# Kernel optimization log

Measured on AMD Instinct MI355X. Metric: run time of the kernel, lower is better.

The kernel has to match this reference:

```python
import jax, jax.numpy as jnp
import numpy as np

D_IN = 2048
D_OUT = 2048
NUM_HEADS = 16
NUM_KV_GROUPS = 4
HEAD_DIM = D_OUT // NUM_HEADS          # 128
GROUP_SIZE = NUM_HEADS // NUM_KV_GROUPS  # 4


def setup_inputs() -> dict:
    key = jax.random.key(0)
    ks = jax.random.split(key, 7)
    B, N = 2, 2048
    s = 1.0 / np.sqrt(D_IN)
    return {
        "query": jax.random.normal(ks[0], (B, N, D_IN), dtype=jnp.float32),
        "key":   jax.random.normal(ks[1], (B, N, D_IN), dtype=jnp.float32),
        "value": jax.random.normal(ks[2], (B, N, D_IN), dtype=jnp.float32),
        # weights stored as (in, out); y = x @ W  (equivalent to torch Linear, no bias)
        "Wq": jax.random.normal(ks[3], (D_IN, D_OUT), dtype=jnp.float32) * s,
        "Wk": jax.random.normal(ks[4], (D_IN, NUM_KV_GROUPS * HEAD_DIM), dtype=jnp.float32) * s,
        "Wv": jax.random.normal(ks[5], (D_IN, NUM_KV_GROUPS * HEAD_DIM), dtype=jnp.float32) * s,
        "Wo": jax.random.normal(ks[6], (D_OUT, D_OUT), dtype=jnp.float32) * s,
    }


def reference(query, key, value, Wq, Wk, Wv, Wo):
    B, N, _ = query.shape
    S = key.shape[1]
    # projections
    q = (query @ Wq).reshape(B, N, NUM_HEADS, HEAD_DIM)        # b n (h g) d
    k = (key   @ Wk).reshape(B, S, NUM_KV_GROUPS, HEAD_DIM)
    v = (value @ Wv).reshape(B, S, NUM_KV_GROUPS, HEAD_DIM)
    # b h n d layouts
    q = q.transpose(0, 2, 1, 3)                                # (B, H, N, d)
    k = k.transpose(0, 2, 1, 3)                                # (B, Hk, S, d)
    v = v.transpose(0, 2, 1, 3)                                # (B, Hk, S, d)
    # rearrange 'b (h g) n d -> b g h n d' with g = GROUP_SIZE, h = NUM_KV_GROUPS
    q = q.reshape(B, NUM_KV_GROUPS, GROUP_SIZE, N, HEAD_DIM).transpose(0, 2, 1, 3, 4)  # (B, g, h, N, d)
    # NOTE: the original module applies NO 1/sqrt(d) scaling — kept faithful.
    scores = jnp.einsum('bghnd,bhsd->bghns', q, k)             # (B, g, h, N, S)
    weights = jax.nn.softmax(scores, axis=-1)                  # dropout p=0.0 -> identity
    ctx = jnp.einsum('bghns,bhsd->bghnd', weights, v)          # (B, g, h, N, d)
    ctx = ctx.transpose(0, 3, 1, 2, 4).reshape(B, N, D_OUT)    # b n (g h d)
    attn_output = ctx @ Wo
    attn_output_weights = weights.reshape(B * NUM_HEADS, N, S) # (b g h) t s
    return attn_output, attn_output_weights
```

## Files before the change

### kernel.cpp

```cpp
#include <hip/hip_runtime.h>
#include <hip/hip_bf16.h>
#include <stdint.h>


typedef __attribute__((ext_vector_type(4))) float f32x4;
typedef __attribute__((ext_vector_type(8))) short short8;

#define GLDS(gsrc, ldst) __builtin_amdgcn_global_load_lds( \
  (const __attribute__((address_space(1))) void*)(gsrc),   \
  (__attribute__((address_space(3))) void*)(ldst), 16, 0, 0)

__device__ __forceinline__ f32x4 MFMA(short8 a, short8 b, f32x4 c) {
  return __builtin_amdgcn_mfma_f32_16x16x32_bf16(a, b, c, 0, 0, 0);
}

__device__ __forceinline__ unsigned short f2bf(float f) {
  union { float f; uint32_t u; } v; v.f = f;
  uint32_t r = v.u + 0x7FFFu + ((v.u >> 16) & 1u);
  return (unsigned short)(r >> 16);
}
__device__ __forceinline__ float bf2f(unsigned short h) {
  union { uint32_t u; float f; } v; v.u = ((uint32_t)h) << 16;
  return v.f;
}
__device__ __forceinline__ int swz128(int r, int byte) {
  return r * 128 + (byte ^ ((r & 7) << 4));
}
__device__ __forceinline__ int swz256(int r, int byte) {
  return r * 256 + ((byte & 15) | ((((byte >> 4) & 15) ^ (r & 15)) << 4));
}

__global__ __launch_bounds__(1024) void transpose_split(
    const float* __restrict__ W, unsigned short* __restrict__ Thi,
    unsigned short* __restrict__ Tlo, int K, int C) {
  __shared__ float tile[32][33];
  int c0 = blockIdx.x * 32, k0 = blockIdx.y * 32;
  int tx = threadIdx.x, ty = threadIdx.y;
  tile[ty][tx] = W[(size_t)(k0 + ty) * C + c0 + tx];
  __syncthreads();
  float f = tile[tx][ty];
  size_t o = (size_t)(c0 + ty) * K + k0 + tx;
  unsigned short hi = f2bf(f);
  Thi[o] = hi;
  if (Tlo) Tlo[o] = f2bf(f - bf2f(hi));
}

template <int MODE>
__global__ __launch_bounds__(256, 2) void proj_kernel(
    const float* __restrict__ X,
    const unsigned short* __restrict__ WTh,
    const unsigned short* __restrict__ WTl,
    unsigned short* __restrict__ Oh,
    unsigned short* __restrict__ Ol,
    int Ctot) {
  __shared__ __align__(16) unsigned short xh[128 * 64];
  __shared__ __align__(16) unsigned short xl[128 * 64];
  __shared__ __align__(16) unsigned short wh[128 * 64];
  __shared__ __align__(16) unsigned short wl[128 * 64];
  const int t = threadIdx.x;
  const int n0 = blockIdx.x * 128, m0 = blockIdx.y * 128;
  const int wid = t >> 6, lane = t & 63;
  const int wm = (wid >> 1) * 64, wn = (wid & 1) * 64;
  f32x4 acc[4][4] = {};
  for (int k0 = 0; k0 < 2048; k0 += 64) {
    #pragma unroll
    for (int i = 0; i < 8; ++i) {
      int e = (i * 256 + t) * 4;
      int r = e >> 6, c = e & 63;
      float4 f = *(const float4*)(X + (size_t)(m0 + r) * 2048 + k0 + c);
      unsigned short h0 = f2bf(f.x), h1 = f2bf(f.y), h2 = f2bf(f.z), h3 = f2bf(f.w);
      int off = swz128(r, c * 2);
      *(uint2*)((char*)xh + off) = make_uint2((unsigned)h0 | ((unsigned)h1 << 16),
                                              (unsigned)h2 | ((unsigned)h3 << 16));
      if (MODE == 0) {
        unsigned short l0 = f2bf(f.x - bf2f(h0)), l1 = f2bf(f.y - bf2f(h1));
        unsigned short l2 = f2bf(f.z - bf2f(h2)), l3 = f2bf(f.w - bf2f(h3));
        *(uint2*)((char*)xl + off) = make_uint2((unsigned)l0 | ((unsigned)l1 << 16),
                                                (unsigned)l2 | ((unsigned)l3 << 16));
      }
    }
    #pragma unroll
    for (int i = 0; i < 4; ++i) {
      int L = i * 4096 + t * 16;
      int r = L >> 7;
      int ss = ((L >> 4) & 7) ^ (r & 7);
      GLDS(WTh + (size_t)(n0 + r) * 2048 + k0 + ss * 8, (char*)wh + i * 4096 + wid * 1024);
      if (MODE == 0)
        GLDS(WTl + (size_t)(n0 + r) * 2048 + k0 + ss * 8, (char*)wl + i * 4096 + wid * 1024);
    }
    __syncthreads();
    #pragma unroll
    for (int ks = 0; ks < 2; ++ks) {
      const int kb = ks * 64 + (lane >> 4) * 16;
      short8 ah[4], al[4], bh[4], bl[4];
      #pragma unroll
      for (int mi = 0; mi < 4; ++mi) {
        int r = wm + mi * 16 + (lane & 15);
        ah[mi] = *(const short8*)((char*)xh + swz128(r, kb));
        if (MODE == 0) al[mi] = *(const short8*)((char*)xl + swz128(r, kb));
      }
      #pragma unroll
      for (int ni = 0; ni < 4; ++ni) {
        int r = wn + ni * 16 + (lane & 15);
        bh[ni] = *(const short8*)((char*)wh + swz128(r, kb));
        if (MODE == 0) bl[ni] = *(const short8*)((char*)wl + swz128(r, kb));
      }
      #pragma unroll
      for (int mi = 0; mi < 4; ++mi)
        #pragma unroll
        for (int ni = 0; ni < 4; ++ni) {
          acc[mi][ni] = MFMA(ah[mi], bh[ni], acc[mi][ni]);
          if (MODE == 0) {
            acc[mi][ni] = MFMA(al[mi], bh[ni], acc[mi][ni]);
            acc[mi][ni] = MFMA(ah[mi], bl[ni], acc[mi][ni]);
          }
        }
    }
    __syncthreads();
  }
  #pragma unroll
  for (int mi = 0; mi < 4; ++mi)
    #pragma unroll
    for (int ni = 0; ni < 4; ++ni)
      #pragma unroll
      for (int rg = 0; rg < 4; ++rg) {
        int row = m0 + wm + mi * 16 + (lane >> 4) * 4 + rg;
        int col = n0 + wn + ni * 16 + (lane & 15);
        float y = acc[mi][ni][rg];
        if (MODE == 0) {
          unsigned short hi = f2bf(y);
          size_t o = (size_t)row * Ctot + col;
          Oh[o] = hi;
          Ol[o] = f2bf(y - bf2f(hi));
        } else {
          Oh[((size_t)(row >> 11) * 512 + col) * 2048 + (row & 2047)] = f2bf(y);
        }
      }
}

__global__ __launch_bounds__(256, 2) void attn_kernel(
    const unsigned short* __restrict__ Qh, const unsigned short* __restrict__ Ql,
    const unsigned short* __restrict__ Kh, const unsigned short* __restrict__ Kl,
    const unsigned short* __restrict__ VT,
    float* __restrict__ Wout,
    unsigned short* __restrict__ Ctx) {
  __shared__ __align__(16) char lds[65536];
  const int bp = blockIdx.y;
  const int b = bp >> 4, p = bp & 15;
  const int hq = (p & 3) * 4 + (p >> 2);
  const int kv = p & 3;
  const int n0 = blockIdx.x * 128;
  const int t = threadIdx.x, wid = t >> 6, lane = t & 63;
  const int wrow = wid * 32;

  {
    size_t qbase = ((size_t)(b * 2048 + n0)) * 2048 + hq * 128;
    #pragma unroll
    for (int i = 0; i < 8; ++i) {
      int L = i * 4096 + t * 16;
      int r = L >> 8;
      int ss = ((L >> 4) & 15) ^ (r & 15);
      GLDS(Qh + qbase + (size_t)r * 2048 + ss * 8, lds + i * 4096 + wid * 1024);
      GLDS(Ql + qbase + (size_t)r * 2048 + ss * 8, lds + 32768 + i * 4096 + wid * 1024);
    }
  }
  __syncthreads();
  short8 qa_h[2][4], qa_l[2][4];
  #pragma unroll
  for (int mf = 0; mf < 2; ++mf)
    #pragma unroll
    for (int ks = 0; ks < 4; ++ks) {
      int r = wrow + mf * 16 + (lane & 15);
      int byte = ks * 64 + (lane >> 4) * 16;
      qa_h[mf][ks] = *(const short8*)(lds + swz256(r, byte));
      qa_l[mf][ks] = *(const short8*)(lds + 32768 + swz256(r, byte));
    }
  __syncthreads();

  const size_t kbase = (size_t)b * 2048 * 512 + kv * 128;
  float lp[2][4];
  #pragma unroll
  for (int mf = 0; mf < 2; ++mf)
    #pragma unroll
    for (int rg = 0; rg < 4; ++rg) lp[mf][rg] = 0.f;

  for (int s0 = 0; s0 < 2048; s0 += 64) {
    #pragma unroll
    for (int i = 0; i < 4; ++i) {
      int L = i * 4096 + t * 16;
      int r = L >> 8;
      int ss = ((L >> 4) & 15) ^ (r & 15);
      GLDS(Kh + kbase + (size_t)(s0 + r) * 512 + ss * 8, lds + i * 4096 + wid * 1024);
      GLDS(Kl + kbase + (size_t)(s0 + r) * 512 + ss * 8, lds + 16384 + i * 4096 + wid * 1024);
    }
    __syncthreads();
    f32x4 sc[2][4] = {};
    #pragma unroll
    for (int sf = 0; sf < 4; ++sf)
      #pragma unroll
      for (int ks = 0; ks < 4; ++ks) {
        int r = sf * 16 + (lane & 15);
        int byte = ks * 64 + (lane >> 4) * 16;
        short8 bh = *(const short8*)(lds + swz256(r, byte));
        short8 bl = *(const short8*)(lds + 16384 + swz256(r, byte));
        #pragma unroll
        for (int mf = 0; mf < 2; ++mf) {
          sc[mf][sf] = MFMA(qa_h[mf][ks], bh, sc[mf][sf]);
          sc[mf][sf] = MFMA(qa_l[mf][ks], bh, sc[mf][sf]);
          sc[mf][sf] = MFMA(qa_h[mf][ks], bl, sc[mf][sf]);
        }
      }
    #pragma unroll
    for (int mf = 0; mf < 2; ++mf)
      #pragma unroll
      for (int rg = 0; rg < 4; ++rg)
        lp[mf][rg] += __expf(sc[mf][0][rg]) + __expf(sc[mf][1][rg]) +
                      __expf(sc[mf][2][rg]) + __expf(sc[mf][3][rg]);
    __syncthreads();
  }

  float invl[2][4];
  #pragma unroll
  for (int mf = 0; mf < 2; ++mf)
    #pragma unroll
    for (int rg = 0; rg < 4; ++rg) {
      float sm = lp[mf][rg];
      sm += __shfl_xor(sm, 1);
      sm += __shfl_xor(sm, 2);
      sm += __shfl_xor(sm, 4);
      sm += __shfl_xor(sm, 8);
      invl[mf][rg] = 1.0f / sm;
    }

  f32x4 cacc[2][8] = {};
  const size_t vbase = ((size_t)b * 512 + kv * 128) * 2048;
  const size_t wbase = ((size_t)bp * 2048 + n0) * 2048;
  for (int s0 = 0; s0 < 2048; s0 += 64) {
    #pragma unroll
    for (int i = 0; i < 4; ++i) {
      int L = i * 4096 + t * 16;
      int r = L >> 8;
      int ss = ((L >> 4) & 15) ^ (r & 15);
      GLDS(Kh + kbase + (size_t)(s0 + r) * 512 + ss * 8, lds + i * 4096 + wid * 1024);
      GLDS(Kl + kbase + (size_t)(s0 + r) * 512 + ss * 8, lds + 16384 + i * 4096 + wid * 1024);
    }
    #pragma unroll
    for (int i = 0; i < 4; ++i) {
      int L = i * 4096 + t * 16;
      int r = L >> 7;
      int ss = ((L >> 4) & 7) ^ (r & 7);
      GLDS(VT + vbase + (size_t)r * 2048 + s0 + ss * 8, lds + 32768 + i * 4096 + wid * 1024);
    }
    __syncthreads();
    f32x4 sc[2][4] = {};
    #pragma unroll
    for (int sf = 0; sf < 4; ++sf)
      #pragma unroll
      for (int ks = 0; ks < 4; ++ks) {
        int r = sf * 16 + (lane & 15);
        int byte = ks * 64 + (lane >> 4) * 16;
        short8 bh = *(const short8*)(lds + swz256(r, byte));
        short8 bl = *(const short8*)(lds + 16384 + swz256(r, byte));
        #pragma unroll
        for (int mf = 0; mf < 2; ++mf) {
          sc[mf][sf] = MFMA(qa_h[mf][ks], bh, sc[mf][sf]);
          sc[mf][sf] = MFMA(qa_l[mf][ks], bh, sc[mf][sf]);
          sc[mf][sf] = MFMA(qa_h[mf][ks], bl, sc[mf][sf]);
        }
      }
    #pragma unroll
    for (int mf = 0; mf < 2; ++mf)
      #pragma unroll
      for (int sf = 0; sf < 4; ++sf)
        #pragma unroll
        for (int rg = 0; rg < 4; ++rg) {
          float w = __expf(sc[mf][sf][rg]) * invl[mf][rg];
          int lr = mf * 16 + (lane >> 4) * 4 + rg;
          int col = sf * 16 + (lane & 15);
          Wout[wbase + (size_t)(wrow + lr) * 2048 + s0 + col] = w;
          *(unsigned short*)(lds + 49152 + wid * 4096 + swz128(lr, col * 2)) = f2bf(w);
        }
    #pragma unroll
    for (int ks = 0; ks < 2; ++ks) {
      short8 pa[2];
      #pragma unroll
      for (int mf = 0; mf < 2; ++mf)
        pa[mf] = *(const short8*)(lds + 49152 + wid * 4096 +
                                  swz128(mf * 16 + (lane & 15), ks * 64 + (lane >> 4) * 16));
      #pragma unroll
      for (int df = 0; df < 8; ++df) {
        short8 vb = *(const short8*)(lds + 32768 +
                                     swz128(df * 16 + (lane & 15), ks * 64 + (lane >> 4) * 16));
        #pragma unroll
        for (int mf = 0; mf < 2; ++mf)
          cacc[mf][df] = MFMA(pa[mf], vb, cacc[mf][df]);
      }
    }
    __syncthreads();
  }
  #pragma unroll
  for (int mf = 0; mf < 2; ++mf)
    #pragma unroll
    for (int df = 0; df < 8; ++df)
      #pragma unroll
      for (int rg = 0; rg < 4; ++rg) {
        int grow = b * 2048 + n0 + wrow + mf * 16 + (lane >> 4) * 4 + rg;
        int col = p * 128 + df * 16 + (lane & 15);
        Ctx[(size_t)grow * 2048 + col] = f2bf(cacc[mf][df][rg]);
      }
}

__global__ __launch_bounds__(256, 2) void gemm_out(
    const unsigned short* __restrict__ A,
    const unsigned short* __restrict__ BT,
    float* __restrict__ Cout) {
  __shared__ __align__(16) unsigned short ash[128 * 64];
  __shared__ __align__(16) unsigned short bsh[128 * 64];
  const int t = threadIdx.x;
  const int n0 = blockIdx.x * 128, m0 = blockIdx.y * 128;
  const int wid = t >> 6, lane = t & 63;
  const int wm = (wid >> 1) * 64, wn = (wid & 1) * 64;
  f32x4 acc[4][4] = {};
  for (int k0 = 0; k0 < 2048; k0 += 64) {
    #pragma unroll
    for (int i = 0; i < 4; ++i) {
      int L = i * 4096 + t * 16;
      int r = L >> 7;
      int ss = ((L >> 4) & 7) ^ (r & 7);
      GLDS(A + (size_t)(m0 + r) * 2048 + k0 + ss * 8, (char*)ash + i * 4096 + wid * 1024);
      GLDS(BT + (size_t)(n0 + r) * 2048 + k0 + ss * 8, (char*)bsh + i * 4096 + wid * 1024);
    }
    __syncthreads();
    #pragma unroll
    for (int ks = 0; ks < 2; ++ks) {
      const int kb = ks * 64 + (lane >> 4) * 16;
      short8 af[4], bfr[4];
      #pragma unroll
      for (int mi = 0; mi < 4; ++mi)
        af[mi] = *(const short8*)((char*)ash + swz128(wm + mi * 16 + (lane & 15), kb));
      #pragma unroll
      for (int ni = 0; ni < 4; ++ni)
        bfr[ni] = *(const short8*)((char*)bsh + swz128(wn + ni * 16 + (lane & 15), kb));
      #pragma unroll
      for (int mi = 0; mi < 4; ++mi)
        #pragma unroll
        for (int ni = 0; ni < 4; ++ni)
          acc[mi][ni] = MFMA(af[mi], bfr[ni], acc[mi][ni]);
    }
    __syncthreads();
  }
  #pragma unroll
  for (int mi = 0; mi < 4; ++mi)
    #pragma unroll
    for (int ni = 0; ni < 4; ++ni)
      #pragma unroll
      for (int rg = 0; rg < 4; ++rg) {
        int row = m0 + wm + mi * 16 + (lane >> 4) * 4 + rg;
        int col = n0 + wn + ni * 16 + (lane & 15);
        Cout[(size_t)row * 2048 + col] = acc[mi][ni][rg];
      }
}

extern "C" void kernel_launch(void* const* d_in, const int* in_sizes, int n_in,
                              void* d_out, int out_size, void* d_ws, size_t ws_size,
                              hipStream_t stream) {
  const float* query = (const float*)d_in[0];
  const float* key   = (const float*)d_in[1];
  const float* value = (const float*)d_in[2];
  const float* Wq = (const float*)d_in[3];
  const float* Wk = (const float*)d_in[4];
  const float* Wv = (const float*)d_in[5];
  const float* Wo = (const float*)d_in[6];
  float* out = (float*)d_out;
  float* wts = out + 8388608;

  char* ws = (char*)d_ws;
  unsigned short* wqT_h = (unsigned short*)(ws);
  unsigned short* wqT_l = (unsigned short*)(ws + 8388608);
  unsigned short* wkT_h = (unsigned short*)(ws + 16777216);
  unsigned short* wkT_l = (unsigned short*)(ws + 18874368);
  unsigned short* wvT_h = (unsigned short*)(ws + 20971520);
  unsigned short* q_h   = (unsigned short*)(ws + 23068672);
  unsigned short* q_l   = (unsigned short*)(ws + 39845888);
  unsigned short* k_h   = (unsigned short*)(ws + 56623104);
  unsigned short* k_l   = (unsigned short*)(ws + 60817408);
  unsigned short* vT    = (unsigned short*)(ws + 65011712);
  unsigned short* ctxb  = (unsigned short*)(ws);
  unsigned short* woT   = (unsigned short*)(ws + 23068672);

  transpose_split<<<dim3(64, 64), dim3(32, 32), 0, stream>>>(Wq, wqT_h, wqT_l, 2048, 2048);
  transpose_split<<<dim3(16, 64), dim3(32, 32), 0, stream>>>(Wk, wkT_h, wkT_l, 2048, 512);
  transpose_split<<<dim3(16, 64), dim3(32, 32), 0, stream>>>(Wv, wvT_h, (unsigned short*)nullptr, 2048, 512);
  proj_kernel<0><<<dim3(16, 32), dim3(256), 0, stream>>>(query, wqT_h, wqT_l, q_h, q_l, 2048);
  proj_kernel<0><<<dim3(4, 32), dim3(256), 0, stream>>>(key, wkT_h, wkT_l, k_h, k_l, 512);
  proj_kernel<1><<<dim3(4, 32), dim3(256), 0, stream>>>(value, wvT_h, (const unsigned short*)nullptr,
                                                        vT, (unsigned short*)nullptr, 512);
  attn_kernel<<<dim3(16, 32), dim3(256), 0, stream>>>(q_h, q_l, k_h, k_l, vT, wts, ctxb);
  transpose_split<<<dim3(64, 64), dim3(32, 32), 0, stream>>>(Wo, woT, (unsigned short*)nullptr, 2048, 2048);
  gemm_out<<<dim3(16, 32), dim3(256), 0, stream>>>(ctxb, woT, out);
}
```

Baseline: 1.167 ms.

## Pre-convert activations to bf16 hi/lo splits and merge K/V projections

Adds a separate pass that converts the query, key and value fp32 activations into bf16 hi/lo split buffers once, before the projections run. The projection GEMMs can then load their A tiles with async global-to-LDS copies, instead of converting fp32 to bf16 in registers on every K step. Before, each tile of X was re-read and re-converted by every column block. The K and V projections are also merged into one launch with 256 blocks, so the grid fills the device better. The cost is an extra full read and write of the activations and a larger workspace.

```diff
diff --git a/kernel.cpp b/kernel.cpp
--- a/kernel.cpp
+++ b/kernel.cpp
@@ -28,6 +28,29 @@
 }
 __device__ __forceinline__ int swz256(int r, int byte) {
   return r * 256 + ((byte & 15) | ((((byte >> 4) & 15) ^ (r & 15)) << 4));
+}
+
+__global__ __launch_bounds__(256) void convert_split3(
+    const float* __restrict__ q, const float* __restrict__ k,
+    const float* __restrict__ v,
+    unsigned short* __restrict__ qh, unsigned short* __restrict__ ql,
+    unsigned short* __restrict__ kh, unsigned short* __restrict__ kl,
+    unsigned short* __restrict__ vh) {
+  const int seg = blockIdx.x >> 13;
+  const int idx = ((blockIdx.x & 8191) * 256 + threadIdx.x) * 4;
+  const float* src = seg == 0 ? q : seg == 1 ? k : v;
+  float4 f = *(const float4*)(src + idx);
+  unsigned short h0 = f2bf(f.x), h1 = f2bf(f.y), h2 = f2bf(f.z), h3 = f2bf(f.w);
+  unsigned short* Hd = seg == 0 ? qh : seg == 1 ? kh : vh;
+  *(uint2*)(Hd + idx) = make_uint2((unsigned)h0 | ((unsigned)h1 << 16),
+                                   (unsigned)h2 | ((unsigned)h3 << 16));
+  if (seg < 2) {
+    unsigned short l0 = f2bf(f.x - bf2f(h0)), l1 = f2bf(f.y - bf2f(h1));
+    unsigned short l2 = f2bf(f.z - bf2f(h2)), l3 = f2bf(f.w - bf2f(h3));
+    unsigned short* Ld = seg == 0 ? ql : kl;
+    *(uint2*)(Ld + idx) = make_uint2((unsigned)l0 | ((unsigned)l1 << 16),
+                                     (unsigned)l2 | ((unsigned)l3 << 16));
+  }
 }
 
 __global__ __launch_bounds__(1024) void transpose_split(
@@ -45,14 +68,10 @@
   if (Tlo) Tlo[o] = f2bf(f - bf2f(hi));
 }
 
-template <int MODE>
-__global__ __launch_bounds__(256, 2) void proj_kernel(
-    const float* __restrict__ X,
-    const unsigned short* __restrict__ WTh,
-    const unsigned short* __restrict__ WTl,
-    unsigned short* __restrict__ Oh,
-    unsigned short* __restrict__ Ol,
-    int Ctot) {
+__global__ __launch_bounds__(256, 2) void qproj_kernel(
+    const unsigned short* __restrict__ Ah, const unsigned short* __restrict__ Al,
+    const unsigned short* __restrict__ WTh, const unsigned short* __restrict__ WTl,
+    unsigned short* __restrict__ Oh, unsigned short* __restrict__ Ol) {
   __shared__ __align__(16) unsigned short xh[128 * 64];
   __shared__ __align__(16) unsigned short xl[128 * 64];
   __shared__ __align__(16) unsigned short wh[128 * 64];
@@ -64,29 +83,15 @@
   f32x4 acc[4][4] = {};
   for (int k0 = 0; k0 < 2048; k0 += 64) {
     #pragma unroll
-    for (int i = 0; i < 8; ++i) {
-      int e = (i * 256 + t) * 4;
-      int r = e >> 6, c = e & 63;
-      float4 f = *(const float4*)(X + (size_t)(m0 + r) * 2048 + k0 + c);
-      unsigned short h0 = f2bf(f.x), h1 = f2bf(f.y), h2 = f2bf(f.z), h3 = f2bf(f.w);
-      int off = swz128(r, c * 2);
-      *(uint2*)((char*)xh + off) = make_uint2((unsigned)h0 | ((unsigned)h1 << 16),
-                                              (unsigned)h2 | ((unsigned)h3 << 16));
-      if (MODE == 0) {
-        unsigned short l0 = f2bf(f.x - bf2f(h0)), l1 = f2bf(f.y - bf2f(h1));
-        unsigned short l2 = f2bf(f.z - bf2f(h2)), l3 = f2bf(f.w - bf2f(h3));
-        *(uint2*)((char*)xl + off) = make_uint2((unsigned)l0 | ((unsigned)l1 << 16),
-                                                (unsigned)l2 | ((unsigned)l3 << 16));
-      }
-    }
-    #pragma unroll
     for (int i = 0; i < 4; ++i) {
       int L = i * 4096 + t * 16;
       int r = L >> 7;
       int ss = ((L >> 4) & 7) ^ (r & 7);
-      GLDS(WTh + (size_t)(n0 + r) * 2048 + k0 + ss * 8, (char*)wh + i * 4096 + wid * 1024);
-      if (MODE == 0)
-        GLDS(WTl + (size_t)(n0 + r) * 2048 + k0 + ss * 8, (char*)wl + i * 4096 + wid * 1024);
+      int dst = i * 4096 + wid * 1024;
+      GLDS(Ah  + (size_t)(m0 + r) * 2048 + k0 + ss * 8, (char*)xh + dst);
+      GLDS(Al  + (size_t)(m0 + r) * 2048 + k0 + ss * 8, (char*)xl + dst);
+      GLDS(WTh + (size_t)(n0 + r) * 2048 + k0 + ss * 8, (char*)wh + dst);
+      GLDS(WTl + (size_t)(n0 + r) * 2048 + k0 + ss * 8, (char*)wl + dst);
     }
     __syncthreads();
     #pragma unroll
@@ -97,23 +102,21 @@
       for (int mi = 0; mi < 4; ++mi) {
         int r = wm + mi * 16 + (lane & 15);
         ah[mi] = *(const short8*)((char*)xh + swz128(r, kb));
-        if (MODE == 0) al[mi] = *(const short8*)((char*)xl + swz128(r, kb));
+        al[mi] = *(const short8*)((char*)xl + swz128(r, kb));
       }
       #pragma unroll
       for (int ni = 0; ni < 4; ++ni) {
         int r = wn + ni * 16 + (lane & 15);
         bh[ni] = *(const short8*)((char*)wh + swz128(r, kb));
-        if (MODE == 0) bl[ni] = *(const short8*)((char*)wl + swz128(r, kb));
+        bl[ni] = *(const short8*)((char*)wl + swz128(r, kb));
       }
       #pragma unroll
       for (int mi = 0; mi < 4; ++mi)
         #pragma unroll
         for (int ni = 0; ni < 4; ++ni) {
           acc[mi][ni] = MFMA(ah[mi], bh[ni], acc[mi][ni]);
-          if (MODE == 0) {
-            acc[mi][ni] = MFMA(al[mi], bh[ni], acc[mi][ni]);
-            acc[mi][ni] = MFMA(ah[mi], bl[ni], acc[mi][ni]);
-          }
+          acc[mi][ni] = MFMA(al[mi], bh[ni], acc[mi][ni]);
+          acc[mi][ni] = MFMA(ah[mi], bl[ni], acc[mi][ni]);
         }
     }
     __syncthreads();
@@ -127,13 +130,93 @@
         int row = m0 + wm + mi * 16 + (lane >> 4) * 4 + rg;
         int col = n0 + wn + ni * 16 + (lane & 15);
         float y = acc[mi][ni][rg];
-        if (MODE == 0) {
+        unsigned short hi = f2bf(y);
+        size_t o = (size_t)row * 2048 + col;
+        Oh[o] = hi;
+        Ol[o] = f2bf(y - bf2f(hi));
+      }
+}
+
+__global__ __launch_bounds__(256, 2) void kv_proj(
+    const unsigned short* __restrict__ kxh, const unsigned short* __restrict__ kxl,
+    const unsigned short* __restrict__ vxh,
+    const unsigned short* __restrict__ wkh, const unsigned short* __restrict__ wkl,
+    const unsigned short* __restrict__ wvh,
+    unsigned short* __restrict__ koh, unsigned short* __restrict__ kol,
+    unsigned short* __restrict__ vot) {
+  __shared__ __align__(16) unsigned short xh[128 * 64];
+  __shared__ __align__(16) unsigned short xl[128 * 64];
+  __shared__ __align__(16) unsigned short wh[128 * 64];
+  __shared__ __align__(16) unsigned short wl[128 * 64];
+  const bool isK = blockIdx.x < 4;
+  const int n0 = (isK ? blockIdx.x : blockIdx.x - 4) * 128;
+  const int m0 = blockIdx.y * 128;
+  const unsigned short* Ah = isK ? kxh : vxh;
+  const unsigned short* Bh = isK ? wkh : wvh;
+  const int t = threadIdx.x;
+  const int wid = t >> 6, lane = t & 63;
+  const int wm = (wid >> 1) * 64, wn = (wid & 1) * 64;
+  f32x4 acc[4][4] = {};
+  for (int k0 = 0; k0 < 2048; k0 += 64) {
+    #pragma unroll
+    for (int i = 0; i < 4; ++i) {
+      int L = i * 4096 + t * 16;
+      int r = L >> 7;
+      int ss = ((L >> 4) & 7) ^ (r & 7);
+      int dst = i * 4096 + wid * 1024;
+      GLDS(Ah + (size_t)(m0 + r) * 2048 + k0 + ss * 8, (char*)xh + dst);
+      GLDS(Bh + (size_t)(n0 + r) * 2048 + k0 + ss * 8, (char*)wh + dst);
+      if (isK) {
+        GLDS(kxl + (size_t)(m0 + r) * 2048 + k0 + ss * 8, (char*)xl + dst);
+        GLDS(wkl + (size_t)(n0 + r) * 2048 + k0 + ss * 8, (char*)wl + dst);
+      }
+    }
+    __syncthreads();
+    #pragma unroll
+    for (int ks = 0; ks < 2; ++ks) {
+      const int kb = ks * 64 + (lane >> 4) * 16;
+      short8 ah[4], al[4], bh[4], bl[4];
+      #pragma unroll
+      for (int mi = 0; mi < 4; ++mi) {
+        int r = wm + mi * 16 + (lane & 15);
+        ah[mi] = *(const short8*)((char*)xh + swz128(r, kb));
+        if (isK) al[mi] = *(const short8*)((char*)xl + swz128(r, kb));
+      }
+      #pragma unroll
+      for (int ni = 0; ni < 4; ++ni) {
+        int r = wn + ni * 16 + (lane & 15);
+        bh[ni] = *(const short8*)((char*)wh + swz128(r, kb));
+        if (isK) bl[ni] = *(const short8*)((char*)wl + swz128(r, kb));
+      }
+      #pragma unroll
+      for (int mi = 0; mi < 4; ++mi)
+        #pragma unroll
+        for (int ni = 0; ni < 4; ++ni) {
+          acc[mi][ni] = MFMA(ah[mi], bh[ni], acc[mi][ni]);
+          if (isK) {
+            acc[mi][ni] = MFMA(al[mi], bh[ni], acc[mi][ni]);
+            acc[mi][ni] = MFMA(ah[mi], bl[ni], acc[mi][ni]);
+          }
+        }
+    }
+    __syncthreads();
+  }
+  #pragma unroll
+  for (int mi = 0; mi < 4; ++mi)
+    #pragma unroll
+    for (int ni = 0; ni < 4; ++ni)
+      #pragma unroll
+      for (int rg = 0; rg < 4; ++rg) {
+        int row = m0 + wm + mi * 16 + (lane >> 4) * 4 + rg;
+        int col = n0 + wn + ni * 16 + (lane & 15);
+        float y = acc[mi][ni][rg];
+        if (isK) {
           unsigned short hi = f2bf(y);
-          size_t o = (size_t)row * Ctot + col;
-          Oh[o] = hi;
-          Ol[o] = f2bf(y - bf2f(hi));
+          size_t o = (size_t)row * 512 + col;
+          koh[o] = hi;
+          kol[o] = f2bf(y - bf2f(hi));
         } else {
-          Oh[((size_t)(row >> 11) * 512 + col) * 2048 + (row & 2047)] = f2bf(y);
+          vot[((size_t)(row >> 11) * 512 + col) * 2048 + (row & 2047)] = f2bf(y);
         }
       }
 }
@@ -385,16 +468,22 @@
   unsigned short* k_h   = (unsigned short*)(ws + 56623104);
   unsigned short* k_l   = (unsigned short*)(ws + 60817408);
   unsigned short* vT    = (unsigned short*)(ws + 65011712);
+  unsigned short* qx_h  = (unsigned short*)(ws + 69206016);
+  unsigned short* qx_l  = (unsigned short*)(ws + 85983232);
+  unsigned short* kx_h  = (unsigned short*)(ws + 102760448);
+  unsigned short* kx_l  = (unsigned short*)(ws + 119537664);
+  unsigned short* vx_h  = (unsigned short*)(ws + 136314880);
   unsigned short* ctxb  = (unsigned short*)(ws);
   unsigned short* woT   = (unsigned short*)(ws + 23068672);
 
+  convert_split3<<<dim3(24576), dim3(256), 0, stream>>>(query, key, value,
+                                                        qx_h, qx_l, kx_h, kx_l, vx_h);
   transpose_split<<<dim3(64, 64), dim3(32, 32), 0, stream>>>(Wq, wqT_h, wqT_l, 2048, 2048);
   transpose_split<<<dim3(16, 64), dim3(32, 32), 0, stream>>>(Wk, wkT_h, wkT_l, 2048, 512);
   transpose_split<<<dim3(16, 64), dim3(32, 32), 0, stream>>>(Wv, wvT_h, (unsigned short*)nullptr, 2048, 512);
-  proj_kernel<0><<<dim3(16, 32), dim3(256), 0, stream>>>(query, wqT_h, wqT_l, q_h, q_l, 2048);
-  proj_kernel<0><<<dim3(4, 32), dim3(256), 0, stream>>>(key, wkT_h, wkT_l, k_h, k_l, 512);
-  proj_kernel<1><<<dim3(4, 32), dim3(256), 0, stream>>>(value, wvT_h, (const unsigned short*)nullptr,
-                                                        vT, (unsigned short*)nullptr, 512);
+  qproj_kernel<<<dim3(16, 32), dim3(256), 0, stream>>>(qx_h, qx_l, wqT_h, wqT_l, q_h, q_l);
+  kv_proj<<<dim3(8, 32), dim3(256), 0, stream>>>(kx_h, kx_l, vx_h, wkT_h, wkT_l, wvT_h,
+                                                 k_h, k_l, vT);
   attn_kernel<<<dim3(16, 32), dim3(256), 0, stream>>>(q_h, q_l, k_h, k_l, vT, wts, ctxb);
   transpose_split<<<dim3(64, 64), dim3(32, 32), 0, stream>>>(Wo, woT, (unsigned short*)nullptr, 2048, 2048);
   gemm_out<<<dim3(16, 32), dim3(256), 0, stream>>>(ctxb, woT, out);
```

Measured after the change: 1.074 ms. 1.09x faster.
